# Kernel tuning notes

Hardware: AMD Instinct MI355X
Metric: run time of the kernel (lower is better)

The kernel has to match this reference:

```python
import jax, jax.numpy as jnp
import numpy as np

NUM_ENTITIES = 100000
NUM_WALKS = 1000000  # num_entities * walk_count
WALK_LEN = 3
INPUT_DIM = 128
OUTPUT_DIM = 256
NUM_REL2 = 192  # 2 * num_relations (forward + inverse)


def setup_inputs() -> dict:
    key = jax.random.key(0)
    k1, k2, k3, k4, k5 = jax.random.split(key, 5)
    segment_ids = jax.random.randint(k1, (NUM_WALKS,), 0, NUM_ENTITIES)
    walk_ids = jax.random.randint(k2, (NUM_WALKS, WALK_LEN), 0, NUM_REL2)
    rel_emb = jax.random.normal(k3, (NUM_REL2, INPUT_DIM), dtype=jnp.float32)
    weight = jax.random.normal(k4, (INPUT_DIM * WALK_LEN, OUTPUT_DIM), dtype=jnp.float32) * (1.0 / np.sqrt(INPUT_DIM * WALK_LEN))
    bias = jax.random.normal(k5, (OUTPUT_DIM,), dtype=jnp.float32) * 0.01
    return {
        "num_entities": NUM_ENTITIES,
        "segment_ids": segment_ids,
        "walk_ids": walk_ids,
        "rel_emb": rel_emb,
        "weight": weight,
        "bias": bias,
    }


def reference(num_entities, segment_ids, walk_ids, rel_emb, weight, bias):
    # Gather relation embeddings per walk step and concatenate along the walk:
    # [N_walks, L, D] -> [N_walks, L*D]  (torch.cat over the walk in the original)
    n_walks = walk_ids.shape[0]
    walk_vecs = rel_emb[walk_ids].reshape(n_walks, -1)
    # Sparse entity<-walk aggregation (torch.sparse.mm with the COO mapping)
    agg = jax.ops.segment_sum(walk_vecs, segment_ids, num_segments=num_entities)
    counts = jax.ops.segment_sum(jnp.ones((n_walks,), walk_vecs.dtype), segment_ids,
                                 num_segments=num_entities)
    # D = diag(1 / (row_sum + 1)); D @ y
    y = agg / (counts + 1.0)[:, None]
    # weighted=True: dense projection, then bias and activation
    y = y @ weight + bias
    return jax.nn.relu(y)
```

## Files before the change

### kernel.cpp

```cpp
#include <hip/hip_runtime.h>
#include <hip/hip_bf16.h>
#include <stdint.h>


#define OD   256
#define DIM  128
#define LW   3

__global__ void k_precompP(const float* __restrict__ rel_emb, const float* __restrict__ W,
                           ushort* __restrict__ P, uint32_t* __restrict__ counts,
                           int NR, int NE) {
    for (int g = blockIdx.x * 256 + threadIdx.x; g < NE; g += gridDim.x * 256)
        counts[g] = 0u;

    int lr = blockIdx.x;
    int l = lr / NR, r = lr - l * NR;
    __shared__ float re[DIM];
    int t = threadIdx.x;
    if (t < DIM) re[t] = rel_emb[r * DIM + t];
    __syncthreads();
    const float* Wl = W + (size_t)(l * DIM) * OD + t;
    float acc = 0.f;
#pragma unroll 8
    for (int k = 0; k < DIM; ++k) acc = fmaf(re[k], Wl[(size_t)k * OD], acc);
    __hip_bfloat16 h = __float2bfloat16(acc);
    P[(size_t)lr * OD + t] = *(ushort*)&h;
}

__global__ void k_fill(const int* __restrict__ seg, const int* __restrict__ wid,
                       uint32_t* __restrict__ counts, uint32_t* __restrict__ csr,
                       int NW, int SLOT) {
    int w = blockIdx.x * blockDim.x + threadIdx.x;
    if (w >= NW) return;
    int s = seg[w];
    uint32_t r = atomicAdd(&counts[s], 1u);
    if (r < (uint32_t)SLOT) {
        int b = w * LW;
        uint32_t r0 = (uint32_t)wid[b], r1 = (uint32_t)wid[b + 1], r2 = (uint32_t)wid[b + 2];
        csr[(size_t)s * SLOT + r] = r0 | (r1 << 8) | (r2 << 16);
    }
}

__device__ __forceinline__ void acc8(float* acc, uint4 q) {
    acc[0] += __uint_as_float(q.x << 16);
    acc[1] += __uint_as_float(q.x & 0xffff0000u);
    acc[2] += __uint_as_float(q.y << 16);
    acc[3] += __uint_as_float(q.y & 0xffff0000u);
    acc[4] += __uint_as_float(q.z << 16);
    acc[5] += __uint_as_float(q.z & 0xffff0000u);
    acc[6] += __uint_as_float(q.w << 16);
    acc[7] += __uint_as_float(q.w & 0xffff0000u);
}

__global__ __launch_bounds__(256) void k_gather(const uint32_t* __restrict__ counts,
                                                const uint32_t* __restrict__ csr,
                                                const ushort* __restrict__ P,
                                                const float* __restrict__ bias,
                                                float* __restrict__ out,
                                                int NR, int NE, int SLOT) {
    int wave = threadIdx.x >> 6;
    int lane = threadIdx.x & 63;
    int e = blockIdx.x * 4 + wave;
    if (e >= NE) return;
    int half = lane >> 5;
    int c = lane & 31;
    const char* Pb = (const char*)P;
    const uint32_t NR1 = (uint32_t)NR * 512u;
    const uint32_t NR2 = 2u * (uint32_t)NR * 512u;
    uint32_t cnt = counts[e];
    uint32_t n = cnt > (uint32_t)SLOT ? (uint32_t)SLOT : cnt;
    const uint32_t* wl = csr + (size_t)e * SLOT;
    uint32_t laneByte = (uint32_t)c * 16u;
    float acc[8] = {0.f, 0.f, 0.f, 0.f, 0.f, 0.f, 0.f, 0.f};

    uint32_t i = 0;
    for (; i + 2 <= n; i += 2) {
        uint32_t p0 = wl[i], p1 = wl[i + 1];
        uint32_t A0 = (p0 & 255u) * 512u;
        uint32_t A1 = ((p0 >> 8) & 255u) * 512u + NR1;
        uint32_t A2 = ((p0 >> 16) & 255u) * 512u + NR2;
        uint32_t B0 = (p1 & 255u) * 512u;
        uint32_t B1 = ((p1 >> 8) & 255u) * 512u + NR1;
        uint32_t B2 = ((p1 >> 16) & 255u) * 512u + NR2;
        uint32_t o0 = half ? A1 : A0;
        uint32_t o1 = half ? B0 : A2;
        uint32_t o2 = half ? B2 : B1;
        uint4 q0 = *(const uint4*)(Pb + o0 + laneByte);
        uint4 q1 = *(const uint4*)(Pb + o1 + laneByte);
        uint4 q2 = *(const uint4*)(Pb + o2 + laneByte);
        acc8(acc, q0);
        acc8(acc, q1);
        acc8(acc, q2);
    }
    if (i < n) {
        uint32_t p0 = wl[i];
        uint32_t A0 = (p0 & 255u) * 512u;
        uint32_t A1 = ((p0 >> 8) & 255u) * 512u + NR1;
        uint32_t A2 = ((p0 >> 16) & 255u) * 512u + NR2;
        uint32_t o0 = half ? A1 : A0;
        uint4 q0 = *(const uint4*)(Pb + o0 + laneByte);
        acc8(acc, q0);
        if (!half) {
            uint4 q1 = *(const uint4*)(Pb + A2 + laneByte);
            acc8(acc, q1);
        }
    }

#pragma unroll
    for (int k = 0; k < 8; ++k) acc[k] += __shfl_xor(acc[k], 32);

    float inv = 1.f / (float)(cnt + 1u);
    int f4 = c * 2 + half;
    float4 bb = ((const float4*)bias)[f4];
    int ab = half * 4;
    float4 o;
    o.x = fmaxf(fmaf(acc[ab + 0], inv, bb.x), 0.f);
    o.y = fmaxf(fmaf(acc[ab + 1], inv, bb.y), 0.f);
    o.z = fmaxf(fmaf(acc[ab + 2], inv, bb.z), 0.f);
    o.w = fmaxf(fmaf(acc[ab + 3], inv, bb.w), 0.f);
    ((float4*)out)[(size_t)e * 64 + f4] = o;
}

extern "C" void kernel_launch(void* const* d_in, const int* in_sizes, int n_in,
                              void* d_out, int out_size, void* d_ws, size_t ws_size,
                              hipStream_t stream) {
    const int*   seg     = (const int*)d_in[1];
    const int*   wid     = (const int*)d_in[2];
    const float* rel_emb = (const float*)d_in[3];
    const float* weight  = (const float*)d_in[4];
    const float* bias    = (const float*)d_in[5];
    float*       out     = (float*)d_out;

    const int NE = out_size / OD;
    const int NW = in_sizes[1];
    const int NR = in_sizes[3] / DIM;

    char* ws = (char*)d_ws;
    size_t o = 0;
    auto alloc = [&](size_t bytes) { void* p = ws + o; o += (bytes + 15) & ~(size_t)15; return p; };
    ushort*   P      = (ushort*)  alloc((size_t)LW * NR * OD * sizeof(ushort));
    uint32_t* counts = (uint32_t*)alloc((size_t)NE * 4);
    size_t avail = (ws_size > o) ? (ws_size - o) : 0;
    int SLOT = (int)(avail / ((size_t)NE * 4));
    if (SLOT > 40) SLOT = 40;
    if (SLOT < 1) SLOT = 1;
    uint32_t* csr = (uint32_t*)alloc((size_t)NE * SLOT * 4);
    (void)n_in;

    k_precompP<<<LW * NR, 256, 0, stream>>>(rel_emb, weight, P, counts, NR, NE);
    k_fill    <<<(NW + 255) / 256, 256, 0, stream>>>(seg, wid, counts, csr, NW, SLOT);
    k_gather  <<<(NE + 3) / 4, 256, 0, stream>>>(counts, csr, P, bias, out, NR, NE, SLOT);
}
```

Measured before the change: 272.5 us.

## Replace CSR gather with per-entity histogram and MFMA GEMM

```diff
diff --git a/kernel.cpp b/kernel.cpp
--- a/kernel.cpp
+++ b/kernel.cpp
@@ -7,11 +7,18 @@
 #define DIM  128
 #define LW   3
 
+typedef __attribute__((ext_vector_type(8))) short bf16x8;
+typedef __attribute__((ext_vector_type(4))) float f32x4;
+
 __global__ void k_precompP(const float* __restrict__ rel_emb, const float* __restrict__ W,
-                           ushort* __restrict__ P, uint32_t* __restrict__ counts,
-                           int NR, int NE) {
-    for (int g = blockIdx.x * 256 + threadIdx.x; g < NE; g += gridDim.x * 256)
-        counts[g] = 0u;
+                           ushort* __restrict__ P, ushort* __restrict__ PT,
+                           uint4* __restrict__ zbuf, int zn4,
+                           uint32_t* __restrict__ counts, int NE, int NR) {
+    for (int g = blockIdx.x * 256 + threadIdx.x; g < zn4; g += gridDim.x * 256)
+        zbuf[g] = make_uint4(0u, 0u, 0u, 0u);
+    if (counts)
+        for (int g = blockIdx.x * 256 + threadIdx.x; g < NE; g += gridDim.x * 256)
+            counts[g] = 0u;
 
     int lr = blockIdx.x;
     int l = lr / NR, r = lr - l * NR;
@@ -24,7 +31,118 @@
 #pragma unroll 8
     for (int k = 0; k < DIM; ++k) acc = fmaf(re[k], Wl[(size_t)k * OD], acc);
     __hip_bfloat16 h = __float2bfloat16(acc);
-    P[(size_t)lr * OD + t] = *(ushort*)&h;
+    ushort hu = *(ushort*)&h;
+    P[(size_t)lr * OD + t] = hu;
+    PT[(size_t)t * (LW * NR) + lr] = hu;
+}
+
+__global__ void k_hist(const int* __restrict__ seg, const int* __restrict__ wid,
+                       uint32_t* __restrict__ H, int NW, int NR) {
+    int w = blockIdx.x * blockDim.x + threadIdx.x;
+    if (w >= NW) return;
+    int e = seg[w];
+    uint32_t base = (uint32_t)e * (uint32_t)((LW * NR) >> 2);
+    int b = w * LW;
+#pragma unroll
+    for (int l = 0; l < LW; ++l) {
+        int bin = l * NR + wid[b + l];
+        atomicAdd(&H[base + (bin >> 2)], 1u << ((bin & 3) * 8));
+    }
+}
+
+__global__ __launch_bounds__(256, 1) void k_gemm(const uint8_t* __restrict__ H8,
+                                                 const ushort* __restrict__ PT,
+                                                 const float* __restrict__ bias,
+                                                 float* __restrict__ out, int NE) {
+    __shared__ ushort Bs[256 * 200];
+    __shared__ ushort As[128 * 72];
+    __shared__ int rowsum[128];
+    const int t = threadIdx.x;
+    const int w = t >> 6;
+    const int l = t & 63;
+    const int lq = l >> 4;
+    const int l16 = l & 15;
+    const int m0 = blockIdx.x * 128;
+
+    f32x4 acc[2][16];
+#pragma unroll
+    for (int mf = 0; mf < 2; ++mf)
+#pragma unroll
+        for (int nf = 0; nf < 16; ++nf) acc[mf][nf] = (f32x4){0.f, 0.f, 0.f, 0.f};
+    if (t < 128) rowsum[t] = 0;
+
+    for (int p = 0; p < 3; ++p) {
+        for (int it = 0; it < 24; ++it) {
+            int id = t + 256 * it;
+            int col = id / 24, c16 = id % 24;
+            uint4 v = *(const uint4*)(PT + (size_t)col * 576 + p * 192 + c16 * 8);
+            *(uint4*)&Bs[col * 200 + c16 * 8] = v;
+        }
+        __syncthreads();
+
+        for (int c = 0; c < 3; ++c) {
+#pragma unroll
+            for (int it = 0; it < 2; ++it) {
+                int id = t + 256 * it;
+                int row = id >> 2, c16 = id & 3;
+                uint4 v = *(const uint4*)(H8 + (size_t)(m0 + row) * 576 + p * 192 + c * 64 + c16 * 16);
+                uint32_t wds[4] = {v.x, v.y, v.z, v.w};
+                ushort hs[16];
+                int s = 0;
+#pragma unroll
+                for (int q = 0; q < 4; ++q) {
+                    uint32_t u = wds[q];
+#pragma unroll
+                    for (int bb = 0; bb < 4; ++bb) {
+                        uint32_t byv = (u >> (8 * bb)) & 255u;
+                        s += (int)byv;
+                        __hip_bfloat16 h = __float2bfloat16((float)byv);
+                        hs[q * 4 + bb] = *(ushort*)&h;
+                    }
+                }
+                if (p == 0) atomicAdd(&rowsum[row], s);
+                ushort* dst = &As[row * 72 + c16 * 16];
+                *(uint4*)(dst) = *(uint4*)&hs[0];
+                *(uint4*)(dst + 8) = *(uint4*)&hs[8];
+            }
+            __syncthreads();
+
+#pragma unroll
+            for (int s2 = 0; s2 < 2; ++s2) {
+                bf16x8 a0 = *(const bf16x8*)&As[(w * 32 + l16) * 72 + s2 * 32 + lq * 8];
+                bf16x8 a1 = *(const bf16x8*)&As[(w * 32 + 16 + l16) * 72 + s2 * 32 + lq * 8];
+#pragma unroll
+                for (int nf = 0; nf < 16; ++nf) {
+                    bf16x8 b = *(const bf16x8*)&Bs[(nf * 16 + l16) * 200 + c * 64 + s2 * 32 + lq * 8];
+                    acc[0][nf] = __builtin_amdgcn_mfma_f32_16x16x32_bf16(a0, b, acc[0][nf], 0, 0, 0);
+                    acc[1][nf] = __builtin_amdgcn_mfma_f32_16x16x32_bf16(a1, b, acc[1][nf], 0, 0, 0);
+                }
+            }
+            __syncthreads();
+        }
+    }
+
+    const int wrow = w * 32;
+#pragma unroll
+    for (int mf = 0; mf < 2; ++mf) {
+        float inv[4];
+#pragma unroll
+        for (int i = 0; i < 4; ++i)
+            inv[i] = 1.f / (float)(rowsum[wrow + mf * 16 + lq * 4 + i] + 1);
+#pragma unroll
+        for (int nf = 0; nf < 16; ++nf) {
+            int col = nf * 16 + l16;
+            float bb = bias[col];
+#pragma unroll
+            for (int i = 0; i < 4; ++i) {
+                int grow = m0 + wrow + mf * 16 + lq * 4 + i;
+                if (grow < NE) {
+                    float v = fmaxf(fmaf(acc[mf][nf][i], inv[i], bb), 0.f);
+                    out[(size_t)grow * OD + col] = v;
+                }
+            }
+        }
+    }
 }
 
 __global__ void k_fill(const int* __restrict__ seg, const int* __restrict__ wid,
@@ -134,20 +252,36 @@
     const int NE = out_size / OD;
     const int NW = in_sizes[1];
     const int NR = in_sizes[3] / DIM;
+    const int K  = LW * NR;
 
     char* ws = (char*)d_ws;
     size_t o = 0;
     auto alloc = [&](size_t bytes) { void* p = ws + o; o += (bytes + 15) & ~(size_t)15; return p; };
-    ushort*   P      = (ushort*)  alloc((size_t)LW * NR * OD * sizeof(ushort));
-    uint32_t* counts = (uint32_t*)alloc((size_t)NE * 4);
-    size_t avail = (ws_size > o) ? (ws_size - o) : 0;
-    int SLOT = (int)(avail / ((size_t)NE * 4));
-    if (SLOT > 40) SLOT = 40;
-    if (SLOT < 1) SLOT = 1;
-    uint32_t* csr = (uint32_t*)alloc((size_t)NE * SLOT * 4);
+    ushort* P  = (ushort*)alloc((size_t)K * OD * sizeof(ushort));
+    ushort* PT = (ushort*)alloc((size_t)OD * K * sizeof(ushort));
     (void)n_in;
 
-    k_precompP<<<LW * NR, 256, 0, stream>>>(rel_emb, weight, P, counts, NR, NE);
-    k_fill    <<<(NW + 255) / 256, 256, 0, stream>>>(seg, wid, counts, csr, NW, SLOT);
-    k_gather  <<<(NE + 3) / 4, 256, 0, stream>>>(counts, csr, P, bias, out, NR, NE, SLOT);
-}
+    const int NEpad = ((NE + 127) / 128) * 128;
+    const size_t Hbytes = (size_t)NEpad * K;
+    const bool gemm_ok = (NR == 192) && (ws_size >= o + Hbytes + 64);
+
+    if (gemm_ok) {
+        uint8_t* H = (uint8_t*)alloc(Hbytes);
+        int zn4 = (int)(Hbytes / 16);
+        k_precompP<<<K, 256, 0, stream>>>(rel_emb, weight, P, PT,
+                                          (uint4*)H, zn4, nullptr, NE, NR);
+        k_hist    <<<(NW + 255) / 256, 256, 0, stream>>>(seg, wid, (uint32_t*)H, NW, NR);
+        k_gemm    <<<NEpad / 128, 256, 0, stream>>>(H, PT, bias, out, NE);
+    } else {
+        uint32_t* counts = (uint32_t*)alloc((size_t)NE * 4);
+        size_t avail = (ws_size > o) ? (ws_size - o) : 0;
+        int SLOT = (int)(avail / ((size_t)NE * 4));
+        if (SLOT > 40) SLOT = 40;
+        if (SLOT < 1) SLOT = 1;
+        uint32_t* csr = (uint32_t*)alloc((size_t)NE * SLOT * 4);
+        k_precompP<<<K, 256, 0, stream>>>(rel_emb, weight, P, PT,
+                                          (uint4*)nullptr, 0, counts, NE, NR);
+        k_fill    <<<(NW + 255) / 256, 256, 0, stream>>>(seg, wid, counts, csr, NW, SLOT);
+        k_gather  <<<(NE + 3) / 4, 256, 0, stream>>>(counts, csr, P, bias, out, NR, NE, SLOT);
+    }
+}
```

Measured after the change: 430.8 us. 58.1% more time.
